# Kernel tuning notes

Hardware: AMD Instinct MI355X
Metric: run time of the kernel (lower is better)

The kernel has to match this reference:

```python
import jax, jax.numpy as jnp
import numpy as np

PLAYERS = 8
DMODEL = 256          # cfg.dmodel (per-embedding dim)
DK = 1024             # cfg.dk
WINDOW = 4096         # cfg.window == T here
A_SPACE = 64
DFULL = DMODEL * 2 * PLAYERS   # 4096, the concatenated model dim


def _positional_encoding(T, dmodel):
    # i = 1/10000^(2j/dmodel); pe[:, ::2]=sin(pos*i), pe[:, 1::2]=cos(pos*i)
    i = 1.0 / jnp.power(jnp.float32(10000.0), jnp.arange(0, dmodel, 2, dtype=jnp.float32) / dmodel)
    pos = jnp.arange(T, dtype=jnp.float32)[:, None]
    pe = jnp.zeros((T, dmodel), dtype=jnp.float32)
    pe = pe.at[:, ::2].set(jnp.sin(pos * i))
    pe = pe.at[:, 1::2].set(jnp.cos(pos * i))
    return pe


def setup_inputs() -> dict:
    key = jax.random.key(0)
    ks = jax.random.split(key, 12)
    n_rows = WINDOW * 2 * PLAYERS  # 65536 one-hot rows
    idx = jax.random.randint(ks[0], (n_rows,), 0, PLAYERS + 1)
    obs = jax.nn.one_hot(idx, PLAYERS + 1, dtype=jnp.int32)
    std = 2.0 / (5.0 * DFULL)  # torch.normal(0, var) uses var as std in the source
    return {
        "obs": obs,
        "o_emb": jax.random.normal(ks[1], (PLAYERS + 1, DMODEL), jnp.float32),
        "d_emb": jax.random.normal(ks[2], (PLAYERS + 1, DMODEL), jnp.float32),
        "WQ": jax.random.normal(ks[3], (DFULL, DK), jnp.float32) * std,
        "WK": jax.random.normal(ks[4], (DFULL, DK), jnp.float32) * std,
        "WV": jax.random.normal(ks[5], (DFULL, DK), jnp.float32) * std,
        "WO": jax.random.normal(ks[6], (DK, DK), jnp.float32) * std,
        "Wo_pol": jax.random.normal(ks[7], (A_SPACE, DK), jnp.float32) * 0.02,
        "bo_pol": jnp.zeros((A_SPACE,), jnp.float32),
        "Wd_pol": jax.random.normal(ks[8], (A_SPACE, DK), jnp.float32) * 0.02,
        "bd_pol": jnp.zeros((A_SPACE,), jnp.float32),
        "Wv": jax.random.normal(ks[9], (1, DK), jnp.float32) * 0.02,
        "bv": jnp.zeros((1,), jnp.float32),
    }


def reference(obs, o_emb, d_emb, WQ, WK, WV, WO, Wo_pol, bo_pol, Wd_pol, bd_pol, Wv, bv):
    obs2 = obs.reshape(-1, PLAYERS + 1)
    # torch.where(row == 1)[1] on one-hot rows == argmax
    idx_o = jnp.argmax(obs2[::2], axis=1)   # [T*players]
    idx_d = jnp.argmax(obs2[1::2], axis=1)  # [T*players]
    emb = jnp.concatenate([o_emb[idx_o], d_emb[idx_d]], axis=1)  # [T*players, 2*dmodel]
    x = emb.reshape(-1, DFULL) * jnp.sqrt(jnp.float32(DMODEL))    # [T, DFULL]
    T = x.shape[0]
    x = x + _positional_encoding(T, DFULL)
    q = x @ WQ  # [T, DK]
    k = x @ WK
    v = x @ WV
    att = jax.nn.softmax((q @ k.T) / jnp.sqrt(jnp.float32(DK)), axis=-1)  # [T, T]
    o = (att @ v) @ WO  # [T, DK]
    h = jax.nn.relu(o[-1])  # last position only, [DK]
    o_logits = h @ Wo_pol.T + bo_pol  # [A_SPACE]
    d_logits = h @ Wd_pol.T + bd_pol  # [A_SPACE]
    value = h @ Wv.T + bv             # [1]
    return (o_logits, d_logits, value)
```

## Files before the change

kernel.cpp:

```cpp
#include <hip/hip_runtime.h>
#include <stdint.h>

#define DK      1024
#define NBLK    256
#define NT      1024
#define LOG2_10000 13.287712379549449f

__device__ float g_sarr[4096];
__device__ float g_kq[4096];
__device__ float g_ol[1024];
__device__ float g_q8[2][8][1024];
__device__ float g_ctx8[2][8][1024];
__device__ float g_w8[2][8][160];

__device__ unsigned bar_gc[256];
__device__ unsigned bar_gf[256];
__device__ unsigned bar_m[64];

__device__ __forceinline__ void stg(float* p, float v) {
    __hip_atomic_store(p, v, __ATOMIC_RELAXED, __HIP_MEMORY_SCOPE_AGENT);
}
__device__ __forceinline__ float lda(const float* p) {
    return __hip_atomic_load(p, __ATOMIC_RELAXED, __HIP_MEMORY_SCOPE_AGENT);
}

__device__ __forceinline__ unsigned gbar_arrive(int bid) {
    unsigned fl = 0;
    asm volatile("s_waitcnt vmcnt(0)" ::: "memory");
    __syncthreads();
    if (threadIdx.x == 0) {
        unsigned g = (unsigned)bid & 7u;
        unsigned* gc = &bar_gc[g * 32];
        unsigned* gf = &bar_gf[g * 32];
        fl = __hip_atomic_load(gf, __ATOMIC_RELAXED, __HIP_MEMORY_SCOPE_AGENT);
        unsigned old = __hip_atomic_fetch_add(gc, 1u, __ATOMIC_RELAXED,
                                              __HIP_MEMORY_SCOPE_AGENT);
        if (old == 31u) {
            __hip_atomic_store(gc, 0u, __ATOMIC_RELAXED,
                               __HIP_MEMORY_SCOPE_AGENT);
            unsigned gen = __hip_atomic_load(&bar_m[32], __ATOMIC_RELAXED,
                                             __HIP_MEMORY_SCOPE_AGENT);
            unsigned o2 = __hip_atomic_fetch_add(&bar_m[0], 1u, __ATOMIC_RELAXED,
                                                 __HIP_MEMORY_SCOPE_AGENT);
            if (o2 == 7u) {
                __hip_atomic_store(&bar_m[0], 0u, __ATOMIC_RELAXED,
                                   __HIP_MEMORY_SCOPE_AGENT);
                __hip_atomic_store(&bar_m[32], gen + 1u, __ATOMIC_RELEASE,
                                   __HIP_MEMORY_SCOPE_AGENT);
            } else {
                int gd = 0;
                while (__hip_atomic_load(&bar_m[32], __ATOMIC_RELAXED,
                                         __HIP_MEMORY_SCOPE_AGENT) == gen) {
                    __builtin_amdgcn_s_sleep(1);
                    if (++gd > (1 << 16)) break;
                }
            }
            __hip_atomic_store(gf, fl + 1u, __ATOMIC_RELEASE,
                               __HIP_MEMORY_SCOPE_AGENT);
        }
    }
    return fl;
}

__device__ __forceinline__ void gbar_wait(int bid, unsigned fl) {
    if (threadIdx.x == 0) {
        unsigned g = (unsigned)bid & 7u;
        unsigned* gf = &bar_gf[g * 32];
        int gd = 0;
        while (__hip_atomic_load(gf, __ATOMIC_RELAXED,
                                 __HIP_MEMORY_SCOPE_AGENT) == fl) {
            __builtin_amdgcn_s_sleep(1);
            if (++gd > (1 << 16)) break;
        }
    }
    __syncthreads();
}

__device__ __forceinline__ void gbar(int bid) { gbar_wait(bid, gbar_arrive(bid)); }

__device__ __forceinline__ float4 bred4(float4 a, float* buf, int tid) {
    #pragma unroll
    for (int off = 32; off; off >>= 1) {
        a.x += __shfl_down(a.x, off, 64);
        a.y += __shfl_down(a.y, off, 64);
        a.z += __shfl_down(a.z, off, 64);
        a.w += __shfl_down(a.w, off, 64);
    }
    float4* b4 = (float4*)buf;
    if ((tid & 63) == 0) b4[tid >> 6] = a;
    __syncthreads();
    float4 r = {0.f, 0.f, 0.f, 0.f};
    if (tid == 0) {
        #pragma unroll
        for (int i = 0; i < 16; ++i) {
            float4 t = b4[i];
            r.x += t.x; r.y += t.y; r.z += t.z; r.w += t.w;
        }
    }
    __syncthreads();
    return r;
}

__global__ __launch_bounds__(1024, 4) void fused_k(
        const int*   __restrict__ obs,
        const float* __restrict__ o_emb,  const float* __restrict__ d_emb,
        const float* __restrict__ WQ,     const float* __restrict__ WK,
        const float* __restrict__ WV,     const float* __restrict__ WO,
        const float* __restrict__ Wo_pol, const float* __restrict__ bo_pol,
        const float* __restrict__ Wd_pol, const float* __restrict__ bd_pol,
        const float* __restrict__ Wv,     const float* __restrict__ bv,
        float* __restrict__ out,          char* __restrict__ ws) {
    (void)ws;

    __shared__ __align__(16) float smem[12416];
    float* axpeL = &smem[12288];
    unsigned char* sidx = (unsigned char*)&smem[12304];

    int bid = blockIdx.x, tid = threadIdx.x;
    const int w  = ((bid & 7) << 5) | (bid >> 3);
    const int sh = bid & 7;

    const unsigned genv = __hip_atomic_load(&bar_m[32], __ATOMIC_RELAXED,
                                            __HIP_MEMORY_SCOPE_AGENT);
    const int par = (int)((genv / 6u) & 1u);
    float* q8  = &g_q8[par][0][0];
    float* q8n = &g_q8[par ^ 1][0][0];
    float* c8  = &g_ctx8[par][0][0];
    float* c8n = &g_ctx8[par ^ 1][0][0];
    float* w8  = &g_w8[par][0][0];
    float* w8n = &g_w8[par ^ 1][0][0];

    {
        if (tid < 69) {
            int idx = w * 69 + tid;
            if (idx < 8192)       stg(&q8n[idx], 0.0f);
            else if (idx < 16384) stg(&c8n[idx - 8192], 0.0f);
            else                  stg(&w8n[idx - 16384], 0.0f);
        }
        int* lidx = (int*)&smem[4100];
        float* lx = &smem[4120];
        if (tid < 256) {
            int g = w * 256 + tid;
            const int* r = obs + (size_t)g * 9;
            int id = 0;
            #pragma unroll
            for (int j = 1; j < 9; ++j) id += j * r[j];
            sidx[(tid & ~15) | ((tid & 1) << 3) | ((tid >> 1) & 7)] =
                (unsigned char)id;
        }
        if (tid < 16) {
            const int* rr = obs + (size_t)(65520 + tid) * 9;
            int id2 = 0;
            #pragma unroll
            for (int j = 1; j < 9; ++j) id2 += j * rr[j];
            lidx[(tid & 1) * 8 + (tid >> 1)] = id2;
        }
        __syncthreads();
        if (tid < 16) {
            int c = w * 16 + tid;
            int p = c >> 9, rr = c & 511;
            const float* tab = (rr < 256) ? o_emb : d_emb;
            int slot = (rr < 256) ? p : 8 + p;
            int r2 = rr & 255;
            float e = tab[lidx[slot] * 256 + r2];
            float f = exp2f(-((float)(c & ~1) * (1.0f / 4096.0f)) * LOG2_10000);
            float sv, cv;
            __sincosf(4095.0f * f, &sv, &cv);
            lx[tid] = e * 16.0f + ((c & 1) ? cv : sv);
        }
        __syncthreads();
        int ksub = tid >> 8, n4 = tid & 255;
        const float4* W4 = (const float4*)WQ;
        float4 acc = {0.f, 0.f, 0.f, 0.f};
        #pragma unroll
        for (int kk = 0; kk < 4; ++kk) {
            int k = ksub * 4 + kk;
            float xv = lx[k];
            float4 wv = W4[(size_t)(w * 16 + k) * 256 + n4];
            acc.x += xv * wv.x; acc.y += xv * wv.y;
            acc.z += xv * wv.z; acc.w += xv * wv.w;
        }
        float4* p4 = (float4*)smem;
        p4[ksub * 256 + n4] = acc;
        __syncthreads();
        if (tid < 256) {
            float4 a = p4[tid], b = p4[256 + tid],
                   c2 = p4[512 + tid], d = p4[768 + tid];
            float* dst = &q8[sh * 1024 + tid * 4];
            atomicAdd(dst + 0, a.x + b.x + c2.x + d.x);
            atomicAdd(dst + 1, a.y + b.y + c2.y + d.y);
            atomicAdd(dst + 2, a.z + b.z + c2.z + d.z);
            atomicAdd(dst + 3, a.w + b.w + c2.w + d.w);
        }
    }
    {
        unsigned fl = gbar_arrive(bid);
        float* lemb = &smem[4096];
        float* lfrq = &smem[8724];
        for (int i = tid; i < 2048; i += NT)
            lfrq[i] = exp2f(-((float)(2 * i) * (1.0f / 4096.0f)) * LOG2_10000);
        for (int i = tid; i < 4608; i += NT) {
            int row = i >> 8, r = i & 255;
            lemb[row * 257 + r] = (row < 9) ? o_emb[row * 256 + r]
                                            : d_emb[(row - 9) * 256 + r];
        }
        gbar_wait(bid, fl);
    }

    {
        float* qsum = &smem[10772];
        float t = 0.0f;
        #pragma unroll
        for (int s2 = 0; s2 < 8; ++s2) t += lda(&q8[s2 * 1024 + tid]);
        qsum[tid] = t;
        __syncthreads();
        int wv_ = tid >> 6, lane = tid & 63;
        int cc = w * 16 + wv_;
        const float4* W4 = (const float4*)(WK + (size_t)cc * DK);
        const float4* q4 = (const float4*)qsum;
        float acc = 0.0f;
        #pragma unroll
        for (int i = 0; i < 4; ++i) {
            float4 wvv = W4[i * 64 + lane];
            float4 qq  = q4[i * 64 + lane];
            acc += wvv.x * qq.x + wvv.y * qq.y + wvv.z * qq.z + wvv.w * qq.w;
        }
        #pragma unroll
        for (int off = 32; off; off >>= 1) acc += __shfl_down(acc, off, 64);
        if (lane == 0) stg(&g_kq[cc], acc * (1.0f / 32.0f));
    }
    gbar(bid);

    {
        float* lkq   = smem;
        float* lemb  = &smem[4096];
        float* lfrq  = &smem[8724];
        float* ldot4 = &smem[10772];
        float* lped  = &smem[11348];
        #pragma unroll
        for (int i = 0; i < 4; ++i) {
            int c = tid + NT * i;
            lkq[c] = lda(&g_kq[c]);
        }
        __syncthreads();
        if (tid < 576) {
            int p = tid >> 2, q = tid & 3;
            int sg = p / 9, id = p % 9;
            int base = (sg < 8) ? sg * 512 : (sg - 8) * 512 + 256;
            const float* e = lemb + ((sg < 8) ? id : (9 + id)) * 257;
            float a = 0.0f;
            for (int i = 0; i < 64; ++i) {
                int r = q * 64 + ((i + q * 13) & 63);
                a += e[r] * lkq[base + r];
            }
            ldot4[tid] = a;
        }
        int tt = tid >> 6, sub = tid & 63;
        int t = w * 16 + tt;
        float acc = 0.0f;
        #pragma unroll 4
        for (int jj = 0; jj < 32; ++jj) {
            int jf = jj * 64 + sub;
            float f = lfrq[jf];
            float svv, cvv;
            __sincosf((float)t * f, &svv, &cvv);
            acc += svv * lkq[2 * jf] + cvv * lkq[2 * jf + 1];
        }
        #pragma unroll
        for (int off = 32; off; off >>= 1) acc += __shfl_down(acc, off, 64);
        if (sub == 0) lped[tt] = acc;
        __syncthreads();
        if (tid < 16) {
            int t2 = w * 16 + tid;
            float tot = lped[tid];
            const uint32_t* ip = (const uint32_t*)(sidx + tid * 16);
            uint32_t u0 = ip[0], u1 = ip[1], u2 = ip[2], u3 = ip[3];
            #pragma unroll
            for (int sg = 0; sg < 16; ++sg) {
                uint32_t u = (sg < 4) ? u0 : (sg < 8) ? u1 : (sg < 12) ? u2 : u3;
                int id = (u >> ((sg & 3) * 8)) & 0xFF;
                int p = (sg * 9 + id) * 4;
                tot += 16.0f * (ldot4[p] + ldot4[p + 1] + ldot4[p + 2] + ldot4[p + 3]);
            }
            stg(&g_sarr[t2], tot);
        }
    }
    gbar(bid);

    {
        float* le   = smem;
        float* pss  = &smem[4352];
        float* psc  = &smem[5376];
        float* lh   = &smem[6400];
        float* mred = &smem[6560];
        float sv4[4];
        float mx = -3.4e38f;
        #pragma unroll
        for (int i = 0; i < 4; ++i) {
            float v = lda(&g_sarr[tid + NT * i]);
            sv4[i] = v;
            mx = fmaxf(mx, v);
        }
        #pragma unroll
        for (int off = 32; off; off >>= 1) mx = fmaxf(mx, __shfl_down(mx, off, 64));
        if ((tid & 63) == 0) mred[tid >> 6] = mx;
        __syncthreads();
        float m = mred[0];
        #pragma unroll
        for (int i = 1; i < 16; ++i) m = fmaxf(m, mred[i]);
        #pragma unroll
        for (int i = 0; i < 4; ++i) le[tid + NT * i] = expf(sv4[i] - m);
        if (tid < 144) lh[tid] = 0.0f;
        __syncthreads();
        if (tid < 256) {
            int lt = tid >> 4, seg = tid & 15;
            int id = sidx[lt * 16 + seg];
            atomicAdd(&lh[seg * 9 + id], le[w * 16 + lt]);
        }
        int jl = tid >> 7, ts = tid & 127;
        int j = w * 8 + jl;
        float f = exp2f(-((float)(2 * j) * (1.0f / 4096.0f)) * LOG2_10000);
        float sf, cf;
        __sincosf(f, &sf, &cf);
        int t0 = ts * 32;
        float sv, cv;
        __sincosf((float)t0 * f, &sv, &cv);
        float ss = 0.f, sc = 0.f;
        #pragma unroll
        for (int i = 0; i < 32; ++i) {
            float a = le[t0 + i];
            ss += a * sv; sc += a * cv;
            float ns = sv * cf + cv * sf;
            cv = cv * cf - sv * sf;
            sv = ns;
        }
        pss[tid] = ss; psc[tid] = sc;
        __syncthreads();
        if (tid < 144) atomicAdd(&w8[sh * 160 + tid], lh[tid]);
        if (tid < 512) {
            int m2 = tid >> 6, l = tid & 63;
            float a  = pss[m2 * 128 + l] + pss[m2 * 128 + 64 + l];
            float b2 = psc[m2 * 128 + l] + psc[m2 * 128 + 64 + l];
            #pragma unroll
            for (int off = 32; off; off >>= 1) {
                a  += __shfl_down(a, off, 64);
                b2 += __shfl_down(b2, off, 64);
            }
            if (l == 0) { axpeL[2 * m2] = a; axpeL[2 * m2 + 1] = b2; }
        }
    }
    gbar(bid);

    {
        float* lw  = &smem[4352];
        float* axv = &smem[4512];
        if (tid < 144) {
            float t = 0.0f;
            #pragma unroll
            for (int s2 = 0; s2 < 8; ++s2) t += lda(&w8[s2 * 160 + tid]);
            lw[tid] = t;
        }
        __syncthreads();
        if (tid == 0) {
            float z = 0.0f;
            #pragma unroll
            for (int i = 0; i < 144; ++i) z += lw[i];
            smem[4496] = 16.0f / z;
        }
        if (tid < 16) {
            int c = w * 16 + tid;
            int p = c >> 9, rr = c & 511;
            const float* tab = (rr < 256) ? o_emb : d_emb;
            int slot = (rr < 256) ? p : 8 + p;
            int r2 = rr & 255;
            float a = 0.0f;
            #pragma unroll
            for (int id2 = 0; id2 < 9; ++id2)
                a += lw[slot * 9 + id2] * tab[id2 * 256 + r2];
            axv[tid] = axpeL[tid] + 16.0f * a;
        }
        __syncthreads();
        float iz = smem[4496];
        int ksub = tid >> 8, n4 = tid & 255;
        const float4* WV4 = (const float4*)WV;
        float4 acc = {0.f, 0.f, 0.f, 0.f};
        #pragma unroll
        for (int kk = 0; kk < 4; ++kk) {
            int k = ksub * 4 + kk;
            float av = axv[k];
            float4 wv = WV4[(size_t)(w * 16 + k) * 256 + n4];
            acc.x += av * wv.x; acc.y += av * wv.y;
            acc.z += av * wv.z; acc.w += av * wv.w;
        }
        float4* p4 = (float4*)smem;
        p4[ksub * 256 + n4] = acc;
        __syncthreads();
        if (tid < 256) {
            float4 a = p4[tid], b = p4[256 + tid],
                   c2 = p4[512 + tid], d = p4[768 + tid];
            float* dst = &c8[sh * 1024 + tid * 4];
            atomicAdd(dst + 0, (a.x + b.x + c2.x + d.x) * iz);
            atomicAdd(dst + 1, (a.y + b.y + c2.y + d.y) * iz);
            atomicAdd(dst + 2, (a.z + b.z + c2.z + d.z) * iz);
            atomicAdd(dst + 3, (a.w + b.w + c2.w + d.w) * iz);
        }
    }
    {
        unsigned fl = gbar_arrive(bid);
        float4 wo = ((const float4*)WO)[(size_t)tid * 256 + w];
        ((float4*)&smem[6144])[tid] = wo;
        gbar_wait(bid, fl);
    }

    {
        float cj = 0.0f;
        #pragma unroll
        for (int s2 = 0; s2 < 8; ++s2) cj += lda(&c8[s2 * 1024 + tid]);
        float4 wo = ((float4*)&smem[6144])[tid];
        float4 acc = {cj * wo.x, cj * wo.y, cj * wo.z, cj * wo.w};
        float4 s4 = bred4(acc, &smem[10496], tid);
        if (tid == 0) {
            stg(&g_ol[w * 4 + 0], s4.x); stg(&g_ol[w * 4 + 1], s4.y);
            stg(&g_ol[w * 4 + 2], s4.z); stg(&g_ol[w * 4 + 3], s4.w);
        }
    }
    {
        unsigned fl = gbar_arrive(bid);
        float wvh = 0.0f, bh = 0.0f;
        if (w < 129) {
            const float* Wh;
            if (w < 64)       { Wh = Wo_pol + (size_t)w * DK;        bh = bo_pol[w]; }
            else if (w < 128) { Wh = Wd_pol + (size_t)(w - 64) * DK; bh = bd_pol[w - 64]; }
            else              { Wh = Wv;                              bh = bv[0]; }
            wvh = Wh[tid];
        }
        gbar_wait(bid, fl);

        if (w < 129) {
            float sacc = fmaxf(lda(&g_ol[tid]), 0.0f) * wvh;
            #pragma unroll
            for (int off = 32; off; off >>= 1) sacc += __shfl_down(sacc, off, 64);
            float* red = smem;
            if ((tid & 63) == 0) red[tid >> 6] = sacc;
            __syncthreads();
            if (tid == 0) {
                float tot = bh;
                #pragma unroll
                for (int i = 0; i < 16; ++i) tot += red[i];
                out[w] = tot;
            }
        }
    }
}

extern "C" void kernel_launch(void* const* d_in, const int* in_sizes, int n_in,
                              void* d_out, int out_size, void* d_ws, size_t ws_size,
                              hipStream_t stream) {
    const int*   obs    = (const int*)  d_in[0];
    const float* o_emb  = (const float*)d_in[1];
    const float* d_emb  = (const float*)d_in[2];
    const float* WQ     = (const float*)d_in[3];
    const float* WK     = (const float*)d_in[4];
    const float* WV     = (const float*)d_in[5];
    const float* WO     = (const float*)d_in[6];
    const float* Wo_pol = (const float*)d_in[7];
    const float* bo_pol = (const float*)d_in[8];
    const float* Wd_pol = (const float*)d_in[9];
    const float* bd_pol = (const float*)d_in[10];
    const float* Wv     = (const float*)d_in[11];
    const float* bv     = (const float*)d_in[12];
    float* out = (float*)d_out;
    char* ws   = (char*)d_ws;

    fused_k<<<dim3(NBLK), dim3(NT), 0, stream>>>(
        obs, o_emb, d_emb, WQ, WK, WV, WO,
        Wo_pol, bo_pol, Wd_pol, bd_pol, Wv, bv, out, ws);
}
```

Measured before the change: 157.0 us.

## Use monotonic-target grid barrier, drop softmax max barrier, prefetch weights into registers

Replaces the two-level generation/flag grid barrier with a monotonic counter scheme in which each barrier waits for a global generation to reach a target value. This removes the reset stores and the second-level spin. The separate max-reduction phase before the softmax is dropped: exp is computed directly on the scores and the histogram work is merged, cutting the barrier count from six to five. Slices of WQ, WK, WV and WO are loaded into registers before barriers so their latency overlaps synchronisation. Skipping the max subtraction risks overflow if scores grow large, and the monotonic counters never reset, so they rely on wraparound behaviour over many launches.

```diff
diff --git a/kernel.cpp b/kernel.cpp
--- a/kernel.cpp
+++ b/kernel.cpp
@@ -4,9 +4,10 @@
 #define DK      1024
 #define NBLK    256
 #define NT      1024
+#define NBAR    5u
 #define LOG2_10000 13.287712379549449f
 
-__device__ float g_sarr[4096];
+__device__ float g_e[4096];
 __device__ float g_kq[4096];
 __device__ float g_ol[1024];
 __device__ float g_q8[2][8][1024];
@@ -14,8 +15,8 @@
 __device__ float g_w8[2][8][160];
 
 __device__ unsigned bar_gc[256];
-__device__ unsigned bar_gf[256];
-__device__ unsigned bar_m[64];
+__device__ unsigned bar_gm[32];
+__device__ unsigned bar_gen;
 
 __device__ __forceinline__ void stg(float* p, float v) {
     __hip_atomic_store(p, v, __ATOMIC_RELAXED, __HIP_MEMORY_SCOPE_AGENT);
@@ -24,59 +25,37 @@
     return __hip_atomic_load(p, __ATOMIC_RELAXED, __HIP_MEMORY_SCOPE_AGENT);
 }
 
-__device__ __forceinline__ unsigned gbar_arrive(int bid) {
-    unsigned fl = 0;
+__device__ __forceinline__ void gbar_arrive(int bid, unsigned target) {
     asm volatile("s_waitcnt vmcnt(0)" ::: "memory");
     __syncthreads();
     if (threadIdx.x == 0) {
         unsigned g = (unsigned)bid & 7u;
-        unsigned* gc = &bar_gc[g * 32];
-        unsigned* gf = &bar_gf[g * 32];
-        fl = __hip_atomic_load(gf, __ATOMIC_RELAXED, __HIP_MEMORY_SCOPE_AGENT);
-        unsigned old = __hip_atomic_fetch_add(gc, 1u, __ATOMIC_RELAXED,
-                                              __HIP_MEMORY_SCOPE_AGENT);
-        if (old == 31u) {
-            __hip_atomic_store(gc, 0u, __ATOMIC_RELAXED,
-                               __HIP_MEMORY_SCOPE_AGENT);
-            unsigned gen = __hip_atomic_load(&bar_m[32], __ATOMIC_RELAXED,
-                                             __HIP_MEMORY_SCOPE_AGENT);
-            unsigned o2 = __hip_atomic_fetch_add(&bar_m[0], 1u, __ATOMIC_RELAXED,
-                                                 __HIP_MEMORY_SCOPE_AGENT);
-            if (o2 == 7u) {
-                __hip_atomic_store(&bar_m[0], 0u, __ATOMIC_RELAXED,
+        unsigned old = __hip_atomic_fetch_add(&bar_gc[g * 32], 1u,
+                           __ATOMIC_RELAXED, __HIP_MEMORY_SCOPE_AGENT);
+        if (old == target * 32u - 1u) {
+            unsigned o2 = __hip_atomic_fetch_add(&bar_gm[0], 1u,
+                              __ATOMIC_RELAXED, __HIP_MEMORY_SCOPE_AGENT);
+            if (o2 == target * 8u - 1u)
+                __hip_atomic_store(&bar_gen, target, __ATOMIC_RELEASE,
                                    __HIP_MEMORY_SCOPE_AGENT);
-                __hip_atomic_store(&bar_m[32], gen + 1u, __ATOMIC_RELEASE,
-                                   __HIP_MEMORY_SCOPE_AGENT);
-            } else {
-                int gd = 0;
-                while (__hip_atomic_load(&bar_m[32], __ATOMIC_RELAXED,
-                                         __HIP_MEMORY_SCOPE_AGENT) == gen) {
-                    __builtin_amdgcn_s_sleep(1);
-                    if (++gd > (1 << 16)) break;
-                }
-            }
-            __hip_atomic_store(gf, fl + 1u, __ATOMIC_RELEASE,
-                               __HIP_MEMORY_SCOPE_AGENT);
-        }
-    }
-    return fl;
-}
-
-__device__ __forceinline__ void gbar_wait(int bid, unsigned fl) {
+        }
+    }
+}
+__device__ __forceinline__ void gbar_wait(unsigned target) {
     if (threadIdx.x == 0) {
-        unsigned g = (unsigned)bid & 7u;
-        unsigned* gf = &bar_gf[g * 32];
         int gd = 0;
-        while (__hip_atomic_load(gf, __ATOMIC_RELAXED,
-                                 __HIP_MEMORY_SCOPE_AGENT) == fl) {
+        while (__hip_atomic_load(&bar_gen, __ATOMIC_RELAXED,
+                                 __HIP_MEMORY_SCOPE_AGENT) < target) {
             __builtin_amdgcn_s_sleep(1);
-            if (++gd > (1 << 16)) break;
-        }
-    }
-    __syncthreads();
-}
-
-__device__ __forceinline__ void gbar(int bid) { gbar_wait(bid, gbar_arrive(bid)); }
+            if (++gd > (1 << 17)) break;
+        }
+    }
+    __syncthreads();
+}
+__device__ __forceinline__ void gbar(int bid, unsigned target) {
+    gbar_arrive(bid, target);
+    gbar_wait(target);
+}
 
 __device__ __forceinline__ float4 bred4(float4 a, float* buf, int tid) {
     #pragma unroll
@@ -115,70 +94,79 @@
     __shared__ __align__(16) float smem[12416];
     float* axpeL = &smem[12288];
     unsigned char* sidx = (unsigned char*)&smem[12304];
+    unsigned* sgen = (unsigned*)&smem[12400];
 
     int bid = blockIdx.x, tid = threadIdx.x;
     const int w  = ((bid & 7) << 5) | (bid >> 3);
     const int sh = bid & 7;
-
-    const unsigned genv = __hip_atomic_load(&bar_m[32], __ATOMIC_RELAXED,
-                                            __HIP_MEMORY_SCOPE_AGENT);
-    const int par = (int)((genv / 6u) & 1u);
+    const int lane = tid & 63;
+    const int ksub = tid >> 8, n4 = tid & 255;
+
+    if (tid == 0)
+        *sgen = __hip_atomic_load(&bar_gen, __ATOMIC_RELAXED,
+                                  __HIP_MEMORY_SCOPE_AGENT);
+
+    const float4* WQ4 = (const float4*)WQ;
+    float4 wqr[4];
+    #pragma unroll
+    for (int kk = 0; kk < 4; ++kk)
+        wqr[kk] = WQ4[(size_t)(w * 16 + ksub * 4 + kk) * 256 + n4];
+
+    int*   lidx = (int*)&smem[4100];
+    float* lx   = &smem[4120];
+    if (tid < 256) {
+        int g = w * 256 + tid;
+        const int* r = obs + (size_t)g * 9;
+        int id = 0;
+        #pragma unroll
+        for (int j = 1; j < 9; ++j) id += j * r[j];
+        sidx[(tid & ~15) | ((tid & 1) << 3) | ((tid >> 1) & 7)] =
+            (unsigned char)id;
+    }
+    if (tid < 16) {
+        const int* rr = obs + (size_t)(65520 + tid) * 9;
+        int id2 = 0;
+        #pragma unroll
+        for (int j = 1; j < 9; ++j) id2 += j * rr[j];
+        lidx[(tid & 1) * 8 + (tid >> 1)] = id2;
+    }
+    __syncthreads();
+    const unsigned gen0 = *sgen;
+    const int par = (int)((gen0 / NBAR) & 1u);
     float* q8  = &g_q8[par][0][0];
-    float* q8n = &g_q8[par ^ 1][0][0];
     float* c8  = &g_ctx8[par][0][0];
-    float* c8n = &g_ctx8[par ^ 1][0][0];
     float* w8  = &g_w8[par][0][0];
-    float* w8n = &g_w8[par ^ 1][0][0];
-
-    {
+    {
+        float* q8n = &g_q8[par ^ 1][0][0];
+        float* c8n = &g_ctx8[par ^ 1][0][0];
+        float* w8n = &g_w8[par ^ 1][0][0];
         if (tid < 69) {
             int idx = w * 69 + tid;
             if (idx < 8192)       stg(&q8n[idx], 0.0f);
             else if (idx < 16384) stg(&c8n[idx - 8192], 0.0f);
             else                  stg(&w8n[idx - 16384], 0.0f);
         }
-        int* lidx = (int*)&smem[4100];
-        float* lx = &smem[4120];
-        if (tid < 256) {
-            int g = w * 256 + tid;
-            const int* r = obs + (size_t)g * 9;
-            int id = 0;
-            #pragma unroll
-            for (int j = 1; j < 9; ++j) id += j * r[j];
-            sidx[(tid & ~15) | ((tid & 1) << 3) | ((tid >> 1) & 7)] =
-                (unsigned char)id;
-        }
-        if (tid < 16) {
-            const int* rr = obs + (size_t)(65520 + tid) * 9;
-            int id2 = 0;
-            #pragma unroll
-            for (int j = 1; j < 9; ++j) id2 += j * rr[j];
-            lidx[(tid & 1) * 8 + (tid >> 1)] = id2;
-        }
-        __syncthreads();
-        if (tid < 16) {
-            int c = w * 16 + tid;
-            int p = c >> 9, rr = c & 511;
-            const float* tab = (rr < 256) ? o_emb : d_emb;
-            int slot = (rr < 256) ? p : 8 + p;
-            int r2 = rr & 255;
-            float e = tab[lidx[slot] * 256 + r2];
-            float f = exp2f(-((float)(c & ~1) * (1.0f / 4096.0f)) * LOG2_10000);
-            float sv, cv;
-            __sincosf(4095.0f * f, &sv, &cv);
-            lx[tid] = e * 16.0f + ((c & 1) ? cv : sv);
-        }
-        __syncthreads();
-        int ksub = tid >> 8, n4 = tid & 255;
-        const float4* W4 = (const float4*)WQ;
+    }
+    if (tid < 16) {
+        int c = w * 16 + tid;
+        int p = c >> 9, rr = c & 511;
+        const float* tab = (rr < 256) ? o_emb : d_emb;
+        int slot = (rr < 256) ? p : 8 + p;
+        int r2 = rr & 255;
+        float e = tab[lidx[slot] * 256 + r2];
+        float f = exp2f(-((float)(c & ~1) * (1.0f / 4096.0f)) * LOG2_10000);
+        float sv, cv;
+        __sincosf(4095.0f * f, &sv, &cv);
+        lx[tid] = e * 16.0f + ((c & 1) ? cv : sv);
+    }
+    __syncthreads();
+    {
         float4 acc = {0.f, 0.f, 0.f, 0.f};
         #pragma unroll
         for (int kk = 0; kk < 4; ++kk) {
-            int k = ksub * 4 + kk;
-            float xv = lx[k];
-            float4 wv = W4[(size_t)(w * 16 + k) * 256 + n4];
-            acc.x += xv * wv.x; acc.y += xv * wv.y;
-            acc.z += xv * wv.z; acc.w += xv * wv.w;
+            float xv = lx[ksub * 4 + kk];
+            acc.x += xv * wqr[kk].x; acc.y += xv * wqr[kk].y;
+            acc.z += xv * wqr[kk].z; acc.w += xv * wqr[kk].w;
         }
         float4* p4 = (float4*)smem;
         p4[ksub * 256 + n4] = acc;
@@ -193,8 +181,14 @@
             atomicAdd(dst + 3, a.w + b.w + c2.w + d.w);
         }
     }
-    {
-        unsigned fl = gbar_arrive(bid);
+    float4 wkr[4];
+    {
+        const float4* WKr = (const float4*)(WK + (size_t)(w * 16 + (tid >> 6)) * DK);
+        #pragma unroll
+        for (int i = 0; i < 4; ++i) wkr[i] = WKr[i * 64 + lane];
+    }
+    gbar_arrive(bid, gen0 + 1);
+    {
         float* lemb = &smem[4096];
         float* lfrq = &smem[8724];
         for (int i = tid; i < 2048; i += NT)
@@ -204,8 +198,8 @@
             lemb[row * 257 + r] = (row < 9) ? o_emb[row * 256 + r]
                                             : d_emb[(row - 9) * 256 + r];
         }
-        gbar_wait(bid, fl);
-    }
+    }
+    gbar_wait(gen0 + 1);
 
     {
         float* qsum = &smem[10772];
@@ -214,34 +208,34 @@
         for (int s2 = 0; s2 < 8; ++s2) t += lda(&q8[s2 * 1024 + tid]);
         qsum[tid] = t;
         __syncthreads();
-        int wv_ = tid >> 6, lane = tid & 63;
-        int cc = w * 16 + wv_;
-        const float4* W4 = (const float4*)(WK + (size_t)cc * DK);
         const float4* q4 = (const float4*)qsum;
         float acc = 0.0f;
         #pragma unroll
         for (int i = 0; i < 4; ++i) {
-            float4 wvv = W4[i * 64 + lane];
-            float4 qq  = q4[i * 64 + lane];
-            acc += wvv.x * qq.x + wvv.y * qq.y + wvv.z * qq.z + wvv.w * qq.w;
+            float4 qq = q4[i * 64 + lane];
+            acc += wkr[i].x * qq.x + wkr[i].y * qq.y
+                 + wkr[i].z * qq.z + wkr[i].w * qq.w;
         }
         #pragma unroll
         for (int off = 32; off; off >>= 1) acc += __shfl_down(acc, off, 64);
-        if (lane == 0) stg(&g_kq[cc], acc * (1.0f / 32.0f));
-    }
-    gbar(bid);
+        if (lane == 0) stg(&g_kq[w * 16 + (tid >> 6)], acc * (1.0f / 32.0f));
+    }
+    gbar(bid, gen0 + 2);
 
     {
         float* lkq   = smem;
         float* lemb  = &smem[4096];
         float* lfrq  = &smem[8724];
         float* ldot4 = &smem[10772];
-        float* lped  = &smem[11348];
+        float* le16  = &smem[11360];
+        float* lped  = &smem[11380];
+        float* lh    = &smem[11400];
         #pragma unroll
         for (int i = 0; i < 4; ++i) {
             int c = tid + NT * i;
             lkq[c] = lda(&g_kq[c]);
         }
+        if (tid < 144) lh[tid] = 0.0f;
         __syncthreads();
         if (tid < 576) {
             int p = tid >> 2, q = tid & 3;
@@ -255,23 +249,24 @@
             }
             ldot4[tid] = a;
         }
-        int tt = tid >> 6, sub = tid & 63;
-        int t = w * 16 + tt;
-        float acc = 0.0f;
-        #pragma unroll 4
-        for (int jj = 0; jj < 32; ++jj) {
-            int jf = jj * 64 + sub;
-            float f = lfrq[jf];
-            float svv, cvv;
-            __sincosf((float)t * f, &svv, &cvv);
-            acc += svv * lkq[2 * jf] + cvv * lkq[2 * jf + 1];
-        }
-        #pragma unroll
-        for (int off = 32; off; off >>= 1) acc += __shfl_down(acc, off, 64);
-        if (sub == 0) lped[tt] = acc;
+        {
+            int tt = tid >> 6;
+            int t = w * 16 + tt;
+            float acc = 0.0f;
+            #pragma unroll 4
+            for (int jj = 0; jj < 32; ++jj) {
+                int jf = jj * 64 + lane;
+                float f = lfrq[jf];
+                float svv, cvv;
+                __sincosf((float)t * f, &svv, &cvv);
+                acc += svv * lkq[2 * jf] + cvv * lkq[2 * jf + 1];
+            }
+            #pragma unroll
+            for (int off = 32; off; off >>= 1) acc += __shfl_down(acc, off, 64);
+            if (lane == 0) lped[tt] = acc;
+        }
         __syncthreads();
         if (tid < 16) {
-            int t2 = w * 16 + tid;
             float tot = lped[tid];
             const uint32_t* ip = (const uint32_t*)(sidx + tid * 16);
             uint32_t u0 = ip[0], u1 = ip[1], u2 = ip[2], u3 = ip[3];
@@ -282,61 +277,67 @@
                 int p = (sg * 9 + id) * 4;
                 tot += 16.0f * (ldot4[p] + ldot4[p + 1] + ldot4[p + 2] + ldot4[p + 3]);
             }
-            stg(&g_sarr[t2], tot);
-        }
-    }
-    gbar(bid);
-
-    {
-        float* le   = smem;
-        float* pss  = &smem[4352];
-        float* psc  = &smem[5376];
-        float* lh   = &smem[6400];
-        float* mred = &smem[6560];
-        float sv4[4];
-        float mx = -3.4e38f;
-        #pragma unroll
-        for (int i = 0; i < 4; ++i) {
-            float v = lda(&g_sarr[tid + NT * i]);
-            sv4[i] = v;
-            mx = fmaxf(mx, v);
-        }
-        #pragma unroll
-        for (int off = 32; off; off >>= 1) mx = fmaxf(mx, __shfl_down(mx, off, 64));
-        if ((tid & 63) == 0) mred[tid >> 6] = mx;
-        __syncthreads();
-        float m = mred[0];
-        #pragma unroll
-        for (int i = 1; i < 16; ++i) m = fmaxf(m, mred[i]);
-        #pragma unroll
-        for (int i = 0; i < 4; ++i) le[tid + NT * i] = expf(sv4[i] - m);
-        if (tid < 144) lh[tid] = 0.0f;
+            float e = expf(tot);
+            le16[tid] = e;
+            stg(&g_e[w * 16 + tid], e);
+        }
         __syncthreads();
         if (tid < 256) {
             int lt = tid >> 4, seg = tid & 15;
             int id = sidx[lt * 16 + seg];
-            atomicAdd(&lh[seg * 9 + id], le[w * 16 + lt]);
-        }
-        int jl = tid >> 7, ts = tid & 127;
-        int j = w * 8 + jl;
-        float f = exp2f(-((float)(2 * j) * (1.0f / 4096.0f)) * LOG2_10000);
-        float sf, cf;
-        __sincosf(f, &sf, &cf);
-        int t0 = ts * 32;
-        float sv, cv;
-        __sincosf((float)t0 * f, &sv, &cv);
-        float ss = 0.f, sc = 0.f;
-        #pragma unroll
-        for (int i = 0; i < 32; ++i) {
-            float a = le[t0 + i];
-            ss += a * sv; sc += a * cv;
-            float ns = sv * cf + cv * sf;
-            cv = cv * cf - sv * sf;
-            sv = ns;
-        }
-        pss[tid] = ss; psc[tid] = sc;
+            atomicAdd(&lh[seg * 9 + id], le16[lt]);
+        }
         __syncthreads();
         if (tid < 144) atomicAdd(&w8[sh * 160 + tid], lh[tid]);
+    }
+    gbar(bid, gen0 + 3);
+
+    float4 wvr[4];
+    {
+        const float4* WV4 = (const float4*)WV;
+        #pragma unroll
+        for (int kk = 0; kk < 4; ++kk)
+            wvr[kk] = WV4[(size_t)(w * 16 + ksub * 4 + kk) * 256 + n4];
+    }
+    {
+        float* le  = smem;
+        float* pss = &smem[4352];
+        float* psc = &smem[5376];
+        float* lw  = &smem[6400];
+        float* axv = &smem[6576];
+        #pragma unroll
+        for (int i = 0; i < 4; ++i) {
+            int c = tid + NT * i;
+            le[c] = lda(&g_e[c]);
+        }
+        if (tid < 144) {
+            float s = 0.0f;
+            #pragma unroll
+            for (int s2 = 0; s2 < 8; ++s2) s += lda(&w8[s2 * 160 + tid]);
+            lw[tid] = s;
+        }
+        __syncthreads();
+        {
+            int jl = tid >> 7, ts = tid & 127;
+            int j = w * 8 + jl;
+            float f = exp2f(-((float)(2 * j) * (1.0f / 4096.0f)) * LOG2_10000);
+            float sf, cf;
+            __sincosf(f, &sf, &cf);
+            int t0 = ts * 32;
+            float sv, cv;
+            __sincosf((float)t0 * f, &sv, &cv);
+            float ss = 0.f, sc = 0.f;
+            #pragma unroll
+            for (int i = 0; i < 32; ++i) {
+                float a = le[t0 + i];
+                ss += a * sv; sc += a * cv;
+                float ns = sv * cf + cv * sf;
+                cv = cv * cf - sv * sf;
+                sv = ns;
+            }
+            pss[tid] = ss; psc[tid] = sc;
+        }
+        __syncthreads();
         if (tid < 512) {
             int m2 = tid >> 6, l = tid & 63;
             float a  = pss[m2 * 128 + l] + pss[m2 * 128 + 64 + l];
@@ -348,25 +349,13 @@
             }
             if (l == 0) { axpeL[2 * m2] = a; axpeL[2 * m2 + 1] = b2; }
         }
-    }
-    gbar(bid);
-
-    {
-        float* lw  = &smem[4352];
-        float* axv = &smem[4512];
-        if (tid < 144) {
-            float t = 0.0f;
-            #pragma unroll
-            for (int s2 = 0; s2 < 8; ++s2) t += lda(&w8[s2 * 160 + tid]);
-            lw[tid] = t;
-        }
-        __syncthreads();
         if (tid == 0) {
             float z = 0.0f;
             #pragma unroll
             for (int i = 0; i < 144; ++i) z += lw[i];
-            smem[4496] = 16.0f / z;
-        }
+            smem[6560] = 16.0f / z;
+        }
+        __syncthreads();
         if (tid < 16) {
             int c = w * 16 + tid;
             int p = c >> 9, rr = c & 511;
@@ -380,75 +369,65 @@
             axv[tid] = axpeL[tid] + 16.0f * a;
         }
         __syncthreads();
-        float iz = smem[4496];
-        int ksub = tid >> 8, n4 = tid & 255;
-        const float4* WV4 = (const float4*)WV;
-        float4 acc = {0.f, 0.f, 0.f, 0.f};
-        #pragma unroll
-        for (int kk = 0; kk < 4; ++kk) {
-            int k = ksub * 4 + kk;
-            float av = axv[k];
-            float4 wv = WV4[(size_t)(w * 16 + k) * 256 + n4];
-            acc.x += av * wv.x; acc.y += av * wv.y;
-            acc.z += av * wv.z; acc.w += av * wv.w;
-        }
-        float4* p4 = (float4*)smem;
-        p4[ksub * 256 + n4] = acc;
-        __syncthreads();
-        if (tid < 256) {
-            float4 a = p4[tid], b = p4[256 + tid],
-                   c2 = p4[512 + tid], d = p4[768 + tid];
-            float* dst = &c8[sh * 1024 + tid * 4];
-            atomicAdd(dst + 0, (a.x + b.x + c2.x + d.x) * iz);
-            atomicAdd(dst + 1, (a.y + b.y + c2.y + d.y) * iz);
-            atomicAdd(dst + 2, (a.z + b.z + c2.z + d.z) * iz);
-            atomicAdd(dst + 3, (a.w + b.w + c2.w + d.w) * iz);
-        }
-    }
-    {
-        unsigned fl = gbar_arrive(bid);
-        float4 wo = ((const float4*)WO)[(size_t)tid * 256 + w];
-        ((float4*)&smem[6144])[tid] = wo;
-        gbar_wait(bid, fl);
-    }
+        {
+            float4 acc = {0.f, 0.f, 0.f, 0.f};
+            #pragma unroll
+            for (int kk = 0; kk < 4; ++kk) {
+                float av = axv[ksub * 4 + kk];
+                acc.x += av * wvr[kk].x; acc.y += av * wvr[kk].y;
+                acc.z += av * wvr[kk].z; acc.w += av * wvr[kk].w;
+            }
+            float4* p4 = (float4*)smem;
+            p4[ksub * 256 + n4] = acc;
+            __syncthreads();
+            if (tid < 256) {
+                float iz = smem[6560];
+                float4 a = p4[tid], b = p4[256 + tid],
+                       c2 = p4[512 + tid], d = p4[768 + tid];
+                float* dst = &c8[sh * 1024 + tid * 4];
+                atomicAdd(dst + 0, (a.x + b.x + c2.x + d.x) * iz);
+                atomicAdd(dst + 1, (a.y + b.y + c2.y + d.y) * iz);
+                atomicAdd(dst + 2, (a.z + b.z + c2.z + d.z) * iz);
+                atomicAdd(dst + 3, (a.w + b.w + c2.w + d.w) * iz);
+            }
+        }
+    }
+    float4 wo = ((const float4*)WO)[(size_t)tid * 256 + w];
+    gbar(bid, gen0 + 4);
 
     {
         float cj = 0.0f;
         #pragma unroll
         for (int s2 = 0; s2 < 8; ++s2) cj += lda(&c8[s2 * 1024 + tid]);
-        float4 wo = ((float4*)&smem[6144])[tid];
         float4 acc = {cj * wo.x, cj * wo.y, cj * wo.z, cj * wo.w};
-        float4 s4 = bred4(acc, &smem[10496], tid);
+        float4 s4 = bred4(acc, &smem[1024], tid);
         if (tid == 0) {
             stg(&g_ol[w * 4 + 0], s4.x); stg(&g_ol[w * 4 + 1], s4.y);
             stg(&g_ol[w * 4 + 2], s4.z); stg(&g_ol[w * 4 + 3], s4.w);
         }
     }
-    {
-        unsigned fl = gbar_arrive(bid);
-        float wvh = 0.0f, bh = 0.0f;
-        if (w < 129) {
-            const float* Wh;
-            if (w < 64)       { Wh = Wo_pol + (size_t)w * DK;        bh = bo_pol[w]; }
-            else if (w < 128) { Wh = Wd_pol + (size_t)(w - 64) * DK; bh = bd_pol[w - 64]; }
-            else              { Wh = Wv;                              bh = bv[0]; }
-            wvh = Wh[tid];
-        }
-        gbar_wait(bid, fl);
-
-        if (w < 129) {
-            float sacc = fmaxf(lda(&g_ol[tid]), 0.0f) * wvh;
-            #pragma unroll
-            for (int off = 32; off; off >>= 1) sacc += __shfl_down(sacc, off, 64);
-            float* red = smem;
-            if ((tid & 63) == 0) red[tid >> 6] = sacc;
-            __syncthreads();
-            if (tid == 0) {
-                float tot = bh;
-                #pragma unroll
-                for (int i = 0; i < 16; ++i) tot += red[i];
-                out[w] = tot;
-            }
+    float wvh = 0.0f, bh = 0.0f;
+    if (w < 129) {
+        const float* Wh;
+        if (w < 64)       { Wh = Wo_pol + (size_t)w * DK;        bh = bo_pol[w]; }
+        else if (w < 128) { Wh = Wd_pol + (size_t)(w - 64) * DK; bh = bd_pol[w - 64]; }
+        else              { Wh = Wv;                              bh = bv[0]; }
+        wvh = Wh[tid];
+    }
+    gbar(bid, gen0 + 5);
+
+    if (w < 129) {
+        float sacc = fmaxf(lda(&g_ol[tid]), 0.0f) * wvh;
+        #pragma unroll
+        for (int off = 32; off; off >>= 1) sacc += __shfl_down(sacc, off, 64);
+        float* red = smem;
+        if ((tid & 63) == 0) red[tid >> 6] = sacc;
+        __syncthreads();
+        if (tid == 0) {
+            float tot = bh;
+            #pragma unroll
+            for (int i = 0; i < 16; ++i) tot += red[i];
+            out[w] = tot;
         }
     }
 }
```

After: 148.5 us. 5.4% less time.
